# Kernel optimization log

Hardware: AMD Instinct MI355X
Metric: run time of the kernel (lower is better)

Reference implementation:

```python
import jax, jax.numpy as jnp
import numpy as np

HIDDEN = 4096
NUM_HEADS = 32
HEAD_DIM = 128
NUM_KV_HEADS = 8
KV_GROUPS = NUM_HEADS // NUM_KV_HEADS
ROPE_THETA = 10000.0
SEQ = 2048
BATCH = 1
NEG_INF = -1e9


def fake_quant_int8(x):
    """Per-tensor symmetric int8 fake quantization (absmax scale)."""
    scale = jnp.maximum(jnp.max(jnp.abs(x)) / 127.0, 1e-8)
    q = jnp.clip(jnp.round(x / scale), -127.0, 127.0) * scale
    # straight-through estimator (no-op in fwd-only, keeps code shared)
    return x + jax.lax.stop_gradient(q - x)


def rotate_half(x):
    x1, x2 = jnp.split(x, 2, axis=-1)
    return jnp.concatenate([-x2, x1], axis=-1)


def rope_cos_sin(position_ids):
    inv_freq = 1.0 / (ROPE_THETA ** (jnp.arange(0, HEAD_DIM, 2, dtype=jnp.float32) / HEAD_DIM))
    freqs = position_ids.astype(jnp.float32)[..., None] * inv_freq  # [B,S,HD/2]
    emb = jnp.concatenate([freqs, freqs], axis=-1)                  # [B,S,HD]
    return jnp.cos(emb), jnp.sin(emb)


def setup_inputs() -> dict:
    key = jax.random.key(0)
    k1, k2, k3, k4, k5 = jax.random.split(key, 5)
    hidden_states = jax.random.normal(k1, (BATCH, SEQ, HIDDEN), dtype=jnp.float32)
    causal = jnp.tril(jnp.ones((SEQ, SEQ), dtype=bool))
    attention_mask = jnp.where(causal, 0.0, NEG_INF).astype(jnp.float32)[None, None]  # [1,1,S,S]
    position_ids = jnp.arange(SEQ, dtype=jnp.int64 if jax.config.jax_enable_x64 else jnp.int32)[None, :]
    s = 0.02
    wq = jax.random.normal(k2, (NUM_HEADS * HEAD_DIM, HIDDEN), dtype=jnp.float32) * s
    wk = jax.random.normal(k3, (NUM_KV_HEADS * HEAD_DIM, HIDDEN), dtype=jnp.float32) * s
    wv = jax.random.normal(k4, (NUM_KV_HEADS * HEAD_DIM, HIDDEN), dtype=jnp.float32) * s
    wo = jax.random.normal(k5, (HIDDEN, NUM_HEADS * HEAD_DIM), dtype=jnp.float32) * s
    return {"hidden_states": hidden_states, "attention_mask": attention_mask,
            "position_ids": position_ids, "wq": wq, "wk": wk, "wv": wv, "wo": wo}


def reference(hidden_states, attention_mask, position_ids, wq, wk, wv, wo):
    B, S, _ = hidden_states.shape

    def qlinear(x, w):  # quantized linear: fake-quant act and weight, y = x @ w.T
        return fake_quant_int8(x) @ fake_quant_int8(w).T

    q = qlinear(hidden_states, wq).reshape(B, S, NUM_HEADS, HEAD_DIM).transpose(0, 2, 1, 3)
    k = qlinear(hidden_states, wk).reshape(B, S, NUM_KV_HEADS, HEAD_DIM).transpose(0, 2, 1, 3)
    v = qlinear(hidden_states, wv).reshape(B, S, NUM_KV_HEADS, HEAD_DIM).transpose(0, 2, 1, 3)

    cos, sin = rope_cos_sin(position_ids)      # [B,S,HD]
    cos, sin = cos[:, None], sin[:, None]      # [B,1,S,HD]
    q = q * cos + rotate_half(q) * sin
    k = k * cos + rotate_half(k) * sin

    # repeat_kv: GQA -> full heads
    k = jnp.repeat(k, KV_GROUPS, axis=1)
    v = jnp.repeat(v, KV_GROUPS, axis=1)

    # quantized QK^T
    scores = jnp.einsum('bhqd,bhkd->bhqk', fake_quant_int8(q), fake_quant_int8(k))
    scores = scores * (1.0 / np.sqrt(HEAD_DIM).astype(np.float32))
    scores = scores + attention_mask[:, :, :, :S]
    probs = jax.nn.softmax(scores.astype(jnp.float32), axis=-1).astype(q.dtype)
    # attention_dropout = 0.0 -> identity

    # quantized AV
    attn_out = jnp.einsum('bhqk,bhkd->bhqd', fake_quant_int8(probs), fake_quant_int8(v))
    attn_out = attn_out.transpose(0, 2, 1, 3).reshape(B, S, NUM_HEADS * HEAD_DIM)
    return qlinear(attn_out, wo)
```

## Files before the change

kernel.cpp:

```cpp
#include <hip/hip_runtime.h>
#include <stdint.h>

#define SEQ   2048
#define HID   4096
#define NH    32
#define NKV   8
#define KVDIM 1024
#define KVCAT 2048

typedef int v4i __attribute__((ext_vector_type(4)));

__device__ __forceinline__ float slot_scale(const unsigned* slots, int slot) {
    return fmaxf(__uint_as_float(slots[slot << 5]) / 127.0f, 1e-8f);
}

__device__ __forceinline__ int q8v(float x, float s) {
    int v = (int)rintf(x / s);
    return v < -127 ? -127 : (v > 127 ? 127 : v);
}

__device__ __forceinline__ float fexp2(float x) {
    float r; asm("v_exp_f32 %0, %1" : "=v"(r) : "v"(x)); return r;
}

__device__ __forceinline__ float amax4(const float* __restrict__ p, long v) {
    float4 x = *(const float4*)(p + v * 4);
    return fmaxf(fmaxf(fabsf(x.x), fabsf(x.y)), fmaxf(fabsf(x.z), fabsf(x.w)));
}

__device__ __forceinline__ void block_amax_atomic(float m, unsigned* slots, int slot) {
    __shared__ float sm[4];
    int lane = threadIdx.x & 63, w = threadIdx.x >> 6;
    for (int off = 32; off; off >>= 1) m = fmaxf(m, __shfl_xor(m, off, 64));
    if (lane == 0) sm[w] = m;
    __syncthreads();
    if (threadIdx.x == 0)
        atomicMax(slots + (slot << 5),
                  __float_as_uint(fmaxf(fmaxf(sm[0], sm[1]), fmaxf(sm[2], sm[3]))));
}

#define NV0 ((long)SEQ * HID / 4)
#define NV1 ((long)HID * HID / 4)
#define NV2 ((long)KVDIM * HID / 4)
__global__ void k_absmax5(const float* __restrict__ a0, const float* __restrict__ a1,
                          const float* __restrict__ a2, const float* __restrict__ a3,
                          const float* __restrict__ a4, unsigned* slots) {
    int b = blockIdx.x;
    const float* p; long n; int slot, lb, nb;
    if (b < 342)       { p = a0; n = NV0; slot = 0; lb = b;        nb = 342; }
    else if (b < 1025) { p = a1; n = NV1; slot = 1; lb = b - 342;  nb = 683; }
    else if (b < 1196) { p = a2; n = NV2; slot = 2; lb = b - 1025; nb = 171; }
    else if (b < 1367) { p = a3; n = NV2; slot = 3; lb = b - 1196; nb = 171; }
    else               { p = a4; n = NV1; slot = 4; lb = b - 1367; nb = 681; }
    long str = (long)nb * 256;
    float m = 0.f, m2 = 0.f;
    long v = (long)lb * 256 + threadIdx.x;
    for (; v + str < n; v += 2 * str) {
        m  = fmaxf(m,  amax4(p, v));
        m2 = fmaxf(m2, amax4(p, v + str));
    }
    if (v < n) m = fmaxf(m, amax4(p, v));
    block_amax_atomic(fmaxf(m, m2), slots, slot);
}

__device__ __forceinline__ void qstore4(const float* __restrict__ src, long v,
                                        int8_t* __restrict__ dst, float s) {
    float4 x = *(const float4*)(src + v * 4);
    unsigned pa = (unsigned)(uint8_t)(int8_t)q8v(x.x, s)
                | ((unsigned)(uint8_t)(int8_t)q8v(x.y, s) << 8)
                | ((unsigned)(uint8_t)(int8_t)q8v(x.z, s) << 16)
                | ((unsigned)(uint8_t)(int8_t)q8v(x.w, s) << 24);
    *(unsigned*)(dst + v * 4) = pa;
}

__global__ void k_quant4(const float* __restrict__ a0, const float* __restrict__ a1,
                         const float* __restrict__ a2, const float* __restrict__ a3,
                         int8_t* __restrict__ d0, int8_t* __restrict__ d1,
                         int8_t* __restrict__ d2, int8_t* __restrict__ d3,
                         const unsigned* __restrict__ slots) {
    int b = blockIdx.x;
    const float* p; int8_t* d; long n; int slot, lb, nb;
    if (b < 512)       { p = a0; d = d0; n = NV0; slot = 0; lb = b;        nb = 512; }
    else if (b < 1536) { p = a1; d = d1; n = NV1; slot = 1; lb = b - 512;  nb = 1024; }
    else if (b < 1792) { p = a2; d = d2; n = NV2; slot = 2; lb = b - 1536; nb = 256; }
    else               { p = a3; d = d3; n = NV2; slot = 3; lb = b - 1792; nb = 256; }
    float s = slot_scale(slots, slot);
    long str = (long)nb * 256;
    for (long v = (long)lb * 256 + threadIdx.x; v < n; v += str) qstore4(p, v, d, s);
}

__global__ void k_quant(const float* __restrict__ x, int8_t* __restrict__ q, long nvec,
                        int rshift, long cmaskv, long ld,
                        const unsigned* __restrict__ slots, int slot) {
    float s = slot_scale(slots, slot);
    for (long vid = blockIdx.x * (long)blockDim.x + threadIdx.x; vid < nvec;
         vid += (long)gridDim.x * blockDim.x) {
        long r = vid >> rshift;
        long c = (vid & cmaskv) << 2;
        float4 v = *(const float4*)(x + r * ld + c);
        unsigned pa = (unsigned)(uint8_t)(int8_t)q8v(v.x, s)
                    | ((unsigned)(uint8_t)(int8_t)q8v(v.y, s) << 8)
                    | ((unsigned)(uint8_t)(int8_t)q8v(v.z, s) << 16)
                    | ((unsigned)(uint8_t)(int8_t)q8v(v.w, s) << 24);
        *(unsigned*)(q + vid * 4) = pa;
    }
}

__global__ void k_ropetab(const int* __restrict__ pos, float* __restrict__ ct,
                          float* __restrict__ st) {
    int tid = blockIdx.x * blockDim.x + threadIdx.x;
    if (tid >= SEQ * 64) return;
    int i = tid & 63, s = tid >> 6;
    double inv = 1.0 / pow(10000.0, (double)((float)(2 * i) * (1.0f / 128.0f)));
    float invf = (float)inv;
    float angf = (float)pos[s] * invf;
    double a = (double)angf;
    ct[tid] = (float)cos(a);
    st[tid] = (float)sin(a);
}

__global__ void k_rope(float* __restrict__ x, long ld, int hbits, int total,
                       const float* __restrict__ ct, const float* __restrict__ st,
                       unsigned* slots, int slot) {
    float m = 0.f;
    for (int t = blockIdx.x * blockDim.x + threadIdx.x; t < total;
         t += gridDim.x * blockDim.x) {
        int i4 = t & 15;
        int h = (t >> 4) & ((1 << hbits) - 1);
        int s = t >> (4 + hbits);
        long base = (long)s * ld + h * 128 + i4 * 4;
        float4 a = *(float4*)(x + base);
        float4 b = *(float4*)(x + base + 64);
        float4 c = *(const float4*)(ct + s * 64 + i4 * 4);
        float4 sn = *(const float4*)(st + s * 64 + i4 * 4);
        float4 o0, o1;
        o0.x = a.x * c.x - b.x * sn.x;  o1.x = b.x * c.x + a.x * sn.x;
        o0.y = a.y * c.y - b.y * sn.y;  o1.y = b.y * c.y + a.y * sn.y;
        o0.z = a.z * c.z - b.z * sn.z;  o1.z = b.z * c.z + a.z * sn.z;
        o0.w = a.w * c.w - b.w * sn.w;  o1.w = b.w * c.w + a.w * sn.w;
        *(float4*)(x + base) = o0;
        *(float4*)(x + base + 64) = o1;
        m = fmaxf(m,
            fmaxf(fmaxf(fmaxf(fabsf(o0.x), fabsf(o0.y)), fmaxf(fabsf(o0.z), fabsf(o0.w))),
                  fmaxf(fmaxf(fabsf(o1.x), fabsf(o1.y)), fmaxf(fabsf(o1.z), fabsf(o1.w)))));
    }
    block_amax_atomic(m, slots, slot);
}

__global__ void k_transq(const float* __restrict__ src, long lds_, int8_t* __restrict__ dst,
                         long ldd, const unsigned* __restrict__ slots, int slot) {
    __shared__ float t[32][33];
    float s = slot_scale(slots, slot);
    int bx = blockIdx.x, by = blockIdx.y;
    int tid = threadIdx.x;
    int c = tid & 31, r0 = tid >> 5;
    #pragma unroll
    for (int j = 0; j < 4; j++) {
        int r = r0 + j * 8;
        t[r][c] = src[(long)(by * 32 + r) * lds_ + bx * 32 + c];
    }
    __syncthreads();
    int d = tid >> 3, k4 = (tid & 7) * 4;
    unsigned pa = 0;
    #pragma unroll
    for (int j = 0; j < 4; j++) {
        int iv = q8v(t[k4 + j][d], s);
        pa |= ((unsigned)(uint8_t)(int8_t)iv) << (8 * j);
    }
    *(unsigned*)(dst + (long)(bx * 32 + d) * ldd + by * 32 + k4) = pa;
}

__global__ __launch_bounds__(256) void k_gemm_i8(
    const int8_t* __restrict__ A, const int8_t* __restrict__ B, float* __restrict__ C,
    int M, int N, int K, unsigned* slots,
    int slotA, int slotB, int slotB2, int nsplit, int am_slot, int am_col0) {
    __shared__ int8_t As[128 * 128];
    __shared__ int8_t Bs[128 * 128];
    const v4i vzero = {0, 0, 0, 0};
    int tid = threadIdx.x, lane = tid & 63, wid = tid >> 6;
    int nbx = N >> 7;
    int nwg = gridDim.x, wg = blockIdx.x;
    int cpx = nwg >> 3;
    int swz = (wg & 7) * cpx + (wg >> 3);
    int bm = swz / nbx, bn = swz % nbx;
    long rowA0 = (long)bm * 128, colB0 = (long)bn * 128;
    int wrow = (wid >> 1) * 64, wcol = (wid & 1) * 64;
    v4i acc[4][4];
    #pragma unroll
    for (int m = 0; m < 4; m++)
        #pragma unroll
        for (int n = 0; n < 4; n++) acc[m][n] = vzero;
    for (int kt = 0; kt < K; kt += 128) {
        #pragma unroll
        for (int i = 0; i < 4; i++) {
            int chunk = tid + i * 256;
            int row = chunk >> 3, cc = chunk & 7;
            int sw = (cc ^ (row & 7)) * 16;
            v4i av = *(const v4i*)(A + (rowA0 + row) * K + kt + cc * 16);
            v4i bv = *(const v4i*)(B + (colB0 + row) * K + kt + cc * 16);
            *(v4i*)(As + row * 128 + sw) = av;
            *(v4i*)(Bs + row * 128 + sw) = bv;
        }
        __syncthreads();
        #pragma unroll
        for (int ks = 0; ks < 2; ks++) {
            v4i af[4], bf[4];
            #pragma unroll
            for (int m = 0; m < 4; m++) {
                int row = wrow + m * 16 + (lane & 15);
                af[m] = *(const v4i*)(As + row * 128 + (((ks * 4 + (lane >> 4)) ^ (row & 7)) * 16));
            }
            #pragma unroll
            for (int n = 0; n < 4; n++) {
                int row = wcol + n * 16 + (lane & 15);
                bf[n] = *(const v4i*)(Bs + row * 128 + (((ks * 4 + (lane >> 4)) ^ (row & 7)) * 16));
            }
            #pragma unroll
            for (int m = 0; m < 4; m++)
                #pragma unroll
                for (int n = 0; n < 4; n++)
                    acc[m][n] = __builtin_amdgcn_mfma_i32_16x16x64_i8(af[m], bf[n], acc[m][n], 0, 0, 0);
        }
        __syncthreads();
    }
    float sA = slot_scale(slots, slotA);
    float sB1 = slot_scale(slots, slotB);
    float sB2 = slot_scale(slots, slotB2);
    float am = 0.f;
    #pragma unroll
    for (int m = 0; m < 4; m++) {
        long row0 = rowA0 + wrow + m * 16 + ((lane >> 4) << 2);
        #pragma unroll
        for (int n = 0; n < 4; n++) {
            int col = (int)colB0 + wcol + n * 16 + (lane & 15);
            float sc = sA * ((col < nsplit) ? sB1 : sB2);
            float* cp = C + row0 * N + col;
            #pragma unroll
            for (int r = 0; r < 4; r++) {
                float val = sc * (float)acc[m][n][r];
                cp[(long)r * N] = val;
                if (col >= am_col0) am = fmaxf(am, fabsf(val));
            }
        }
    }
    if (am_slot >= 0) block_amax_atomic(am, slots, am_slot);
}

__global__ __launch_bounds__(256) void k_attn(
    const int8_t* __restrict__ Qq, const int8_t* __restrict__ Kq, const int8_t* __restrict__ Vtq,
    int* __restrict__ AO, unsigned* slots) {
    __shared__ int8_t Qs[64 * 128];
    __shared__ int8_t Ks[64 * 128];
    __shared__ int8_t Vs[128 * 64];
    __shared__ int smx[4];
    const v4i vzero = {0, 0, 0, 0};
    const int NEGS = -(1 << 29);
    int tid = threadIdx.x, lane = tid & 63, w = tid >> 6;
    int qlan = lane & 15, g = lane >> 4;
    int idx = blockIdx.x;
    int qb = 31 - (idx >> 5), h = idx & 31, kvh = h >> 2;
    float sq = slot_scale(slots, 5), sk = slot_scale(slots, 6);
    float c2 = sq * sk * 0.08838834764831845f * 1.4426950408889634f;
    #pragma unroll
    for (int i = 0; i < 2; i++) {
        int chunk = tid + i * 256;
        int row = chunk >> 3, cc = chunk & 7;
        v4i v = *(const v4i*)(Qq + (long)(qb * 64 + row) * HID + h * 128 + cc * 16);
        *(v4i*)(Qs + row * 128 + ((cc ^ (row & 7)) * 16)) = v;
    }
    __syncthreads();
    v4i aq[2];
    #pragma unroll
    for (int ks = 0; ks < 2; ks++) {
        int row = w * 16 + qlan;
        aq[ks] = *(const v4i*)(Qs + row * 128 + (((ks * 4 + g) ^ (row & 7)) * 16));
    }
    int mi = -(1 << 30);
    float l = 0.f;
    for (int kt = 0; kt <= qb; kt++) {
        __syncthreads();
        #pragma unroll
        for (int i = 0; i < 2; i++) {
            int chunk = tid + i * 256;
            int row = chunk >> 3, cc = chunk & 7;
            v4i v = *(const v4i*)(Kq + (long)(kt * 64 + row) * KVDIM + kvh * 128 + cc * 16);
            *(v4i*)(Ks + row * 128 + ((cc ^ (row & 7)) * 16)) = v;
        }
        __syncthreads();
        v4i sf[4] = {vzero, vzero, vzero, vzero};
        #pragma unroll
        for (int ks = 0; ks < 2; ks++)
            #pragma unroll
            for (int f = 0; f < 4; f++) {
                int row = f * 16 + qlan;
                v4i bk = *(const v4i*)(Ks + row * 128 + (((ks * 4 + g) ^ (row & 7)) * 16));
                sf[f] = __builtin_amdgcn_mfma_i32_16x16x64_i8(bk, aq[ks], sf[f], 0, 0, 0);
            }
        int qthr = qb * 64 + w * 16 + qlan - kt * 64;
        int sv[16];
        #pragma unroll
        for (int f = 0; f < 4; f++)
            #pragma unroll
            for (int r = 0; r < 4; r++) {
                int kl = f * 16 + g * 4 + r;
                sv[f * 4 + r] = (kl > qthr) ? NEGS : sf[f][r];
            }
        int tm = sv[0];
        #pragma unroll
        for (int e = 1; e < 16; e++) tm = tm > sv[e] ? tm : sv[e];
        tm = max(tm, __shfl_xor(tm, 16, 64));
        tm = max(tm, __shfl_xor(tm, 32, 64));
        int mn = tm > mi ? tm : mi;
        float esc = fexp2(c2 * (float)(mi - mn));
        float es = 0.f;
        #pragma unroll
        for (int e = 0; e < 16; e++) es += fexp2(c2 * (float)(sv[e] - mn));
        es += __shfl_xor(es, 16, 64);
        es += __shfl_xor(es, 32, 64);
        l = l * esc + es;
        mi = mn;
    }
    float invl = 127.0f / l;
    unsigned* Ps32 = (unsigned*)Qs;
    int pwr = w * 320;
    v4i of[8];
    #pragma unroll
    for (int nf = 0; nf < 8; nf++) of[nf] = vzero;
    for (int kt = 0; kt <= qb; kt++) {
        __syncthreads();
        #pragma unroll
        for (int i = 0; i < 2; i++) {
            int chunk = tid + i * 256;
            int row = chunk >> 3, cc = chunk & 7;
            v4i v = *(const v4i*)(Kq + (long)(kt * 64 + row) * KVDIM + kvh * 128 + cc * 16);
            *(v4i*)(Ks + row * 128 + ((cc ^ (row & 7)) * 16)) = v;
        }
        #pragma unroll
        for (int i = 0; i < 2; i++) {
            int chunk = tid + i * 256;
            int row = chunk >> 2, cc = chunk & 3;
            v4i v = *(const v4i*)(Vtq + (long)(kvh * 128 + row) * SEQ + kt * 64 + cc * 16);
            *(v4i*)(Vs + row * 64 + ((cc ^ (row & 3)) * 16)) = v;
        }
        __syncthreads();
        v4i sf[4] = {vzero, vzero, vzero, vzero};
        #pragma unroll
        for (int ks = 0; ks < 2; ks++)
            #pragma unroll
            for (int f = 0; f < 4; f++) {
                int row = f * 16 + qlan;
                v4i bk = *(const v4i*)(Ks + row * 128 + (((ks * 4 + g) ^ (row & 7)) * 16));
                sf[f] = __builtin_amdgcn_mfma_i32_16x16x64_i8(bk, aq[ks], sf[f], 0, 0, 0);
            }
        int qthr = qb * 64 + w * 16 + qlan - kt * 64;
        #pragma unroll
        for (int f = 0; f < 4; f++) {
            unsigned pk = 0;
            #pragma unroll
            for (int r = 0; r < 4; r++) {
                int kl = f * 16 + g * 4 + r;
                int s = (kl > qthr) ? NEGS : sf[f][r];
                float t = fexp2(c2 * (float)(s - mi));
                int pq = (int)rintf(t * invl);
                pk |= ((unsigned)pq) << (8 * r);
            }
            Ps32[pwr + (4 * f + g) * 20 + qlan] = pk;
        }
        int rb = pwr + 80 * g + qlan;
        v4i ap;
        ap[0] = (int)Ps32[rb];
        ap[1] = (int)Ps32[rb + 20];
        ap[2] = (int)Ps32[rb + 40];
        ap[3] = (int)Ps32[rb + 60];
        #pragma unroll
        for (int nf = 0; nf < 8; nf++) {
            int row = nf * 16 + qlan;
            v4i bv = *(const v4i*)(Vs + row * 64 + ((g ^ (row & 3)) * 16));
            of[nf] = __builtin_amdgcn_mfma_i32_16x16x64_i8(ap, bv, of[nf], 0, 0, 0);
        }
    }
    int mymax = 0;
    #pragma unroll
    for (int nf = 0; nf < 8; nf++)
        #pragma unroll
        for (int r = 0; r < 4; r++) {
            int val = of[nf][r];
            int av = val < 0 ? -val : val;
            mymax = av > mymax ? av : mymax;
            int qg = qb * 64 + w * 16 + 4 * g + r;
            AO[(long)qg * HID + h * 128 + nf * 16 + qlan] = val;
        }
    #pragma unroll
    for (int off = 1; off < 64; off <<= 1) {
        int o2 = __shfl_xor(mymax, off, 64);
        mymax = o2 > mymax ? o2 : mymax;
    }
    if (lane == 0) smx[w] = mymax;
    __syncthreads();
    if (tid == 0) {
        int mm = max(max(smx[0], smx[1]), max(smx[2], smx[3]));
        atomicMax(slots + (8 << 5), (unsigned)mm);
    }
}

__global__ void k_quant_ao(const int* __restrict__ a, int8_t* __restrict__ q, unsigned* slots) {
    float sv = slot_scale(slots, 7);
    float spv = (1.0f / 127.0f) * sv;
    float amax = spv * (float)(int)slots[8 << 5];
    float s = fmaxf(amax / 127.0f, 1e-8f);
    long nvec = (long)SEQ * HID / 4;
    for (long vid = blockIdx.x * (long)blockDim.x + threadIdx.x; vid < nvec;
         vid += (long)gridDim.x * blockDim.x) {
        int4 v = *(const int4*)(a + vid * 4);
        int a0 = q8v(spv * (float)v.x, s);
        int a1 = q8v(spv * (float)v.y, s);
        int a2 = q8v(spv * (float)v.z, s);
        int a3 = q8v(spv * (float)v.w, s);
        unsigned pa = (unsigned)(uint8_t)(int8_t)a0
                    | ((unsigned)(uint8_t)(int8_t)a1 << 8)
                    | ((unsigned)(uint8_t)(int8_t)a2 << 16)
                    | ((unsigned)(uint8_t)(int8_t)a3 << 24);
        *(unsigned*)(q + vid * 4) = pa;
    }
    if (blockIdx.x == 0 && threadIdx.x == 0) slots[9 << 5] = __float_as_uint(amax);
}

extern "C" void kernel_launch(void* const* d_in, const int* in_sizes, int n_in,
                              void* d_out, int out_size, void* d_ws, size_t ws_size,
                              hipStream_t stream) {
    (void)in_sizes; (void)n_in; (void)out_size;
    const float* hid = (const float*)d_in[0];
    const int* pos = (const int*)d_in[2];
    const float* wqp = (const float*)d_in[3];
    const float* wkp = (const float*)d_in[4];
    const float* wvp = (const float*)d_in[5];
    const float* wop = (const float*)d_in[6];
    float* out = (float*)d_out;
    char* ws = (char*)d_ws;

    size_t o = 0;
    auto alloc = [&](size_t sz) { size_t r = o; o += (sz + 255) & ~(size_t)255; return r; };
    unsigned* slots = (unsigned*)(ws + alloc(2048));
    int8_t* Xq   = (int8_t*)(ws + alloc((size_t)SEQ * HID));
    int8_t* Wqq  = (int8_t*)(ws + alloc((size_t)HID * HID));
    int8_t* Wkvq = (int8_t*)(ws + alloc((size_t)KVCAT * HID));
    float*  Qf   = (float*)(ws + alloc((size_t)SEQ * HID * 4));
    float*  KVf  = (float*)(ws + alloc((size_t)SEQ * KVCAT * 4));
    int8_t* Qq   = (int8_t*)(ws + alloc((size_t)SEQ * HID));
    int8_t* Kq   = (int8_t*)(ws + alloc((size_t)SEQ * KVDIM));
    int8_t* Vtq  = (int8_t*)(ws + alloc((size_t)KVDIM * SEQ));
    float*  ctab = (float*)(ws + alloc((size_t)SEQ * 64 * 4));
    float*  stab = (float*)(ws + alloc((size_t)SEQ * 64 * 4));
    if (ws_size < o) return;
    int8_t* Woq = Wqq;
    int*    AOint = (int*)Qf;
    int8_t* AOq = Xq;

    hipMemsetAsync(slots, 0, 2048, stream);
    k_ropetab<<<SEQ * 64 / 256, 256, 0, stream>>>(pos, ctab, stab);
    k_absmax5<<<2048, 256, 0, stream>>>(hid, wqp, wkp, wvp, wop, slots);
    k_quant4<<<2048, 256, 0, stream>>>(hid, wqp, wkp, wvp,
                                       Xq, Wqq, Wkvq, Wkvq + (size_t)KVDIM * HID, slots);
    k_gemm_i8<<<512, 256, 0, stream>>>(Xq, Wqq, Qf, SEQ, HID, HID, slots,
                                       0, 1, 1, 1 << 30, -1, 1 << 30);
    k_gemm_i8<<<256, 256, 0, stream>>>(Xq, Wkvq, KVf, SEQ, KVCAT, HID, slots,
                                       0, 2, 3, KVDIM, 7, KVDIM);
    const long CALL = 0x3FFFFFFFL;
    k_quant<<<2048, 256, 0, stream>>>(wop, Woq, (long)HID * HID / 4, 40, CALL, 0, slots, 4);
    k_rope<<<1024, 256, 0, stream>>>(Qf, HID, 5, SEQ * NH * 16, ctab, stab, slots, 5);
    k_rope<<<1024, 256, 0, stream>>>(KVf, KVCAT, 3, SEQ * NKV * 16, ctab, stab, slots, 6);
    k_quant<<<2048, 256, 0, stream>>>(Qf, Qq, (long)SEQ * HID / 4, 40, CALL, 0, slots, 5);
    k_quant<<<1024, 256, 0, stream>>>(KVf, Kq, (long)SEQ * KVDIM / 4, 8, 255, KVCAT, slots, 6);
    k_transq<<<dim3(32, 64), 256, 0, stream>>>(KVf + KVDIM, KVCAT, Vtq, SEQ, slots, 7);
    k_attn<<<1024, 256, 0, stream>>>(Qq, Kq, Vtq, AOint, slots);
    k_quant_ao<<<2048, 256, 0, stream>>>(AOint, AOq, slots);
    k_gemm_i8<<<512, 256, 0, stream>>>(AOq, Woq, out, SEQ, HID, HID, slots,
                                       9, 4, 4, 1 << 30, -1, 1 << 30);
}
```

Baseline: 350.8 us.

## Double-buffer GEMM and attention tiles with direct global-to-LDS async loads

Replaces the register-staged global-to-LDS copies in the int8 GEMM and the attention kernel with global_load_lds direct transfers. Tiles are double-buffered so the next K/V (or A/B) tile loads while MFMAs run on the current one. The attention kernel also applies the causal mask only on the diagonal tile and raises wave priority around the MFMA sections. This doubles LDS use (64 KB in the GEMM), which may lower occupancy, and relies on vmcnt waits for correctness.

```diff
diff --git a/kernel.cpp b/kernel.cpp
--- a/kernel.cpp
+++ b/kernel.cpp
@@ -9,6 +9,14 @@
 #define KVCAT 2048
 
 typedef int v4i __attribute__((ext_vector_type(4)));
+
+#define VMCNT0 asm volatile("s_waitcnt vmcnt(0)" ::: "memory")
+
+__device__ __forceinline__ void gload16(const void* g, void* l) {
+    __builtin_amdgcn_global_load_lds(
+        (const __attribute__((address_space(1))) void*)(uintptr_t)g,
+        (__attribute__((address_space(3))) void*)(uintptr_t)l, 16, 0, 0);
+}
 
 __device__ __forceinline__ float slot_scale(const unsigned* slots, int slot) {
     return fmaxf(__uint_as_float(slots[slot << 5]) / 127.0f, 1e-8f);
@@ -174,8 +182,8 @@
     const int8_t* __restrict__ A, const int8_t* __restrict__ B, float* __restrict__ C,
     int M, int N, int K, unsigned* slots,
     int slotA, int slotB, int slotB2, int nsplit, int am_slot, int am_col0) {
-    __shared__ int8_t As[128 * 128];
-    __shared__ int8_t Bs[128 * 128];
+    __shared__ int8_t As[2][128 * 128];
+    __shared__ int8_t Bs[2][128 * 128];
     const v4i vzero = {0, 0, 0, 0};
     int tid = threadIdx.x, lane = tid & 63, wid = tid >> 6;
     int nbx = N >> 7;
@@ -185,35 +193,36 @@
     int bm = swz / nbx, bn = swz % nbx;
     long rowA0 = (long)bm * 128, colB0 = (long)bn * 128;
     int wrow = (wid >> 1) * 64, wcol = (wid & 1) * 64;
+    int lr = lane >> 3;
+    int swc = ((lane & 7) ^ lr) * 16;
+    const int8_t* ga = A + (rowA0 + wid * 8 + lr) * (long)K + swc;
+    const int8_t* gb = B + (colB0 + wid * 8 + lr) * (long)K + swc;
     v4i acc[4][4];
     #pragma unroll
     for (int m = 0; m < 4; m++)
         #pragma unroll
         for (int n = 0; n < 4; n++) acc[m][n] = vzero;
-    for (int kt = 0; kt < K; kt += 128) {
+
+    auto STAGE = [&](int buf, int kt) {
         #pragma unroll
         for (int i = 0; i < 4; i++) {
-            int chunk = tid + i * 256;
-            int row = chunk >> 3, cc = chunk & 7;
-            int sw = (cc ^ (row & 7)) * 16;
-            v4i av = *(const v4i*)(A + (rowA0 + row) * K + kt + cc * 16);
-            v4i bv = *(const v4i*)(B + (colB0 + row) * K + kt + cc * 16);
-            *(v4i*)(As + row * 128 + sw) = av;
-            *(v4i*)(Bs + row * 128 + sw) = bv;
-        }
-        __syncthreads();
+            gload16(ga + kt + (long)(i * 32) * K, &As[buf][(wid * 8 + i * 32) * 128]);
+            gload16(gb + kt + (long)(i * 32) * K, &Bs[buf][(wid * 8 + i * 32) * 128]);
+        }
+    };
+    auto COMPUTE = [&](int buf) {
         #pragma unroll
         for (int ks = 0; ks < 2; ks++) {
             v4i af[4], bf[4];
             #pragma unroll
             for (int m = 0; m < 4; m++) {
                 int row = wrow + m * 16 + (lane & 15);
-                af[m] = *(const v4i*)(As + row * 128 + (((ks * 4 + (lane >> 4)) ^ (row & 7)) * 16));
+                af[m] = *(const v4i*)(&As[buf][row * 128 + (((ks * 4 + (lane >> 4)) ^ (row & 7)) * 16)]);
             }
             #pragma unroll
             for (int n = 0; n < 4; n++) {
                 int row = wcol + n * 16 + (lane & 15);
-                bf[n] = *(const v4i*)(Bs + row * 128 + (((ks * 4 + (lane >> 4)) ^ (row & 7)) * 16));
+                bf[n] = *(const v4i*)(&Bs[buf][row * 128 + (((ks * 4 + (lane >> 4)) ^ (row & 7)) * 16)]);
             }
             #pragma unroll
             for (int m = 0; m < 4; m++)
@@ -221,8 +230,21 @@
                 for (int n = 0; n < 4; n++)
                     acc[m][n] = __builtin_amdgcn_mfma_i32_16x16x64_i8(af[m], bf[n], acc[m][n], 0, 0, 0);
         }
+    };
+
+    STAGE(0, 0);
+    VMCNT0;
+    __syncthreads();
+    int nt = K >> 7, cur = 0;
+    for (int t = 0; t < nt - 1; t++) {
+        STAGE(cur ^ 1, (t + 1) << 7);
+        COMPUTE(cur);
+        VMCNT0;
         __syncthreads();
-    }
+        cur ^= 1;
+    }
+    COMPUTE(cur);
+
     float sA = slot_scale(slots, slotA);
     float sB1 = slot_scale(slots, slotB);
     float sB2 = slot_scale(slots, slotB2);
@@ -250,8 +272,8 @@
     const int8_t* __restrict__ Qq, const int8_t* __restrict__ Kq, const int8_t* __restrict__ Vtq,
     int* __restrict__ AO, unsigned* slots) {
     __shared__ int8_t Qs[64 * 128];
-    __shared__ int8_t Ks[64 * 128];
-    __shared__ int8_t Vs[128 * 64];
+    __shared__ int8_t Ks[2][64 * 128];
+    __shared__ int8_t Vs[2][128 * 64];
     __shared__ int smx[4];
     const v4i vzero = {0, 0, 0, 0};
     const int NEGS = -(1 << 29);
@@ -261,50 +283,69 @@
     int qb = 31 - (idx >> 5), h = idx & 31, kvh = h >> 2;
     float sq = slot_scale(slots, 5), sk = slot_scale(slots, 6);
     float c2 = sq * sk * 0.08838834764831845f * 1.4426950408889634f;
-    #pragma unroll
-    for (int i = 0; i < 2; i++) {
-        int chunk = tid + i * 256;
-        int row = chunk >> 3, cc = chunk & 7;
-        v4i v = *(const v4i*)(Qq + (long)(qb * 64 + row) * HID + h * 128 + cc * 16);
-        *(v4i*)(Qs + row * 128 + ((cc ^ (row & 7)) * 16)) = v;
-    }
+    int lr8 = lane >> 3;
+    int swc = ((lane & 7) ^ lr8) * 16;
+    int lr4 = lane >> 2;
+    int vswc = ((lane & 3) ^ (lr4 & 3)) * 16;
+    const int8_t* kbase = Kq + ((long)(w * 8 + lr8)) * KVDIM + kvh * 128 + swc;
+    const int8_t* vbase = Vtq + ((long)kvh * 128 + w * 16 + lr4) * SEQ + vswc;
+    auto STAGE_K = [&](int buf, int kt) {
+        #pragma unroll
+        for (int i = 0; i < 2; i++)
+            gload16(kbase + ((long)kt * 64 + i * 32) * KVDIM, &Ks[buf][(w * 8 + i * 32) * 128]);
+    };
+    auto STAGE_V = [&](int buf, int kt) {
+        #pragma unroll
+        for (int i = 0; i < 2; i++)
+            gload16(vbase + (long)(i * 64) * SEQ + kt * 64, &Vs[buf][(w * 16 + i * 64) * 64]);
+    };
+    {
+        const int8_t* qbase = Qq + ((long)qb * 64 + w * 8 + lr8) * HID + h * 128 + swc;
+        #pragma unroll
+        for (int i = 0; i < 2; i++)
+            gload16(qbase + (long)(i * 32) * HID, &Qs[(w * 8 + i * 32) * 128]);
+    }
+    STAGE_K(0, 0);
+    VMCNT0;
     __syncthreads();
     v4i aq[2];
     #pragma unroll
     for (int ks = 0; ks < 2; ks++) {
         int row = w * 16 + qlan;
-        aq[ks] = *(const v4i*)(Qs + row * 128 + (((ks * 4 + g) ^ (row & 7)) * 16));
+        aq[ks] = *(const v4i*)(&Qs[row * 128 + (((ks * 4 + g) ^ (row & 7)) * 16)]);
     }
     int mi = -(1 << 30);
     float l = 0.f;
+    int buf = 0;
     for (int kt = 0; kt <= qb; kt++) {
-        __syncthreads();
-        #pragma unroll
-        for (int i = 0; i < 2; i++) {
-            int chunk = tid + i * 256;
-            int row = chunk >> 3, cc = chunk & 7;
-            v4i v = *(const v4i*)(Kq + (long)(kt * 64 + row) * KVDIM + kvh * 128 + cc * 16);
-            *(v4i*)(Ks + row * 128 + ((cc ^ (row & 7)) * 16)) = v;
-        }
-        __syncthreads();
+        if (kt < qb) STAGE_K(buf ^ 1, kt + 1);
         v4i sf[4] = {vzero, vzero, vzero, vzero};
+        __builtin_amdgcn_s_setprio(1);
         #pragma unroll
         for (int ks = 0; ks < 2; ks++)
             #pragma unroll
             for (int f = 0; f < 4; f++) {
                 int row = f * 16 + qlan;
-                v4i bk = *(const v4i*)(Ks + row * 128 + (((ks * 4 + g) ^ (row & 7)) * 16));
+                v4i bk = *(const v4i*)(&Ks[buf][row * 128 + (((ks * 4 + g) ^ (row & 7)) * 16)]);
                 sf[f] = __builtin_amdgcn_mfma_i32_16x16x64_i8(bk, aq[ks], sf[f], 0, 0, 0);
             }
-        int qthr = qb * 64 + w * 16 + qlan - kt * 64;
+        __builtin_amdgcn_s_setprio(0);
         int sv[16];
-        #pragma unroll
-        for (int f = 0; f < 4; f++)
-            #pragma unroll
-            for (int r = 0; r < 4; r++) {
-                int kl = f * 16 + g * 4 + r;
-                sv[f * 4 + r] = (kl > qthr) ? NEGS : sf[f][r];
-            }
+        if (kt == qb) {
+            int qthr = w * 16 + qlan;
+            #pragma unroll
+            for (int f = 0; f < 4; f++)
+                #pragma unroll
+                for (int r = 0; r < 4; r++) {
+                    int kl = f * 16 + g * 4 + r;
+                    sv[f * 4 + r] = (kl > qthr) ? NEGS : sf[f][r];
+                }
+        } else {
+            #pragma unroll
+            for (int f = 0; f < 4; f++)
+                #pragma unroll
+                for (int r = 0; r < 4; r++) sv[f * 4 + r] = sf[f][r];
+        }
         int tm = sv[0];
         #pragma unroll
         for (int e = 1; e < 16; e++) tm = tm > sv[e] ? tm : sv[e];
@@ -319,6 +360,9 @@
         es += __shfl_xor(es, 32, 64);
         l = l * esc + es;
         mi = mn;
+        VMCNT0;
+        __syncthreads();
+        buf ^= 1;
     }
     float invl = 127.0f / l;
     unsigned* Ps32 = (unsigned*)Qs;
@@ -326,45 +370,51 @@
     v4i of[8];
     #pragma unroll
     for (int nf = 0; nf < 8; nf++) of[nf] = vzero;
+    STAGE_K(0, 0);
+    STAGE_V(0, 0);
+    VMCNT0;
+    __syncthreads();
+    buf = 0;
     for (int kt = 0; kt <= qb; kt++) {
-        __syncthreads();
-        #pragma unroll
-        for (int i = 0; i < 2; i++) {
-            int chunk = tid + i * 256;
-            int row = chunk >> 3, cc = chunk & 7;
-            v4i v = *(const v4i*)(Kq + (long)(kt * 64 + row) * KVDIM + kvh * 128 + cc * 16);
-            *(v4i*)(Ks + row * 128 + ((cc ^ (row & 7)) * 16)) = v;
-        }
-        #pragma unroll
-        for (int i = 0; i < 2; i++) {
-            int chunk = tid + i * 256;
-            int row = chunk >> 2, cc = chunk & 3;
-            v4i v = *(const v4i*)(Vtq + (long)(kvh * 128 + row) * SEQ + kt * 64 + cc * 16);
-            *(v4i*)(Vs + row * 64 + ((cc ^ (row & 3)) * 16)) = v;
-        }
-        __syncthreads();
+        if (kt < qb) { STAGE_K(buf ^ 1, kt + 1); STAGE_V(buf ^ 1, kt + 1); }
         v4i sf[4] = {vzero, vzero, vzero, vzero};
+        __builtin_amdgcn_s_setprio(1);
         #pragma unroll
         for (int ks = 0; ks < 2; ks++)
             #pragma unroll
             for (int f = 0; f < 4; f++) {
                 int row = f * 16 + qlan;
-                v4i bk = *(const v4i*)(Ks + row * 128 + (((ks * 4 + g) ^ (row & 7)) * 16));
+                v4i bk = *(const v4i*)(&Ks[buf][row * 128 + (((ks * 4 + g) ^ (row & 7)) * 16)]);
                 sf[f] = __builtin_amdgcn_mfma_i32_16x16x64_i8(bk, aq[ks], sf[f], 0, 0, 0);
             }
-        int qthr = qb * 64 + w * 16 + qlan - kt * 64;
-        #pragma unroll
-        for (int f = 0; f < 4; f++) {
-            unsigned pk = 0;
-            #pragma unroll
-            for (int r = 0; r < 4; r++) {
-                int kl = f * 16 + g * 4 + r;
-                int s = (kl > qthr) ? NEGS : sf[f][r];
-                float t = fexp2(c2 * (float)(s - mi));
-                int pq = (int)rintf(t * invl);
-                pk |= ((unsigned)pq) << (8 * r);
-            }
-            Ps32[pwr + (4 * f + g) * 20 + qlan] = pk;
+        __builtin_amdgcn_s_setprio(0);
+        if (kt == qb) {
+            int qthr = w * 16 + qlan;
+            #pragma unroll
+            for (int f = 0; f < 4; f++) {
+                unsigned pk = 0;
+                #pragma unroll
+                for (int r = 0; r < 4; r++) {
+                    int kl = f * 16 + g * 4 + r;
+                    int s = (kl > qthr) ? NEGS : sf[f][r];
+                    float t = fexp2(c2 * (float)(s - mi));
+                    int pq = (int)rintf(t * invl);
+                    pk |= ((unsigned)pq) << (8 * r);
+                }
+                Ps32[pwr + (4 * f + g) * 20 + qlan] = pk;
+            }
+        } else {
+            #pragma unroll
+            for (int f = 0; f < 4; f++) {
+                unsigned pk = 0;
+                #pragma unroll
+                for (int r = 0; r < 4; r++) {
+                    float t = fexp2(c2 * (float)(sf[f][r] - mi));
+                    int pq = (int)rintf(t * invl);
+                    pk |= ((unsigned)pq) << (8 * r);
+                }
+                Ps32[pwr + (4 * f + g) * 20 + qlan] = pk;
+            }
         }
         int rb = pwr + 80 * g + qlan;
         v4i ap;
@@ -372,12 +422,17 @@
         ap[1] = (int)Ps32[rb + 20];
         ap[2] = (int)Ps32[rb + 40];
         ap[3] = (int)Ps32[rb + 60];
+        __builtin_amdgcn_s_setprio(1);
         #pragma unroll
         for (int nf = 0; nf < 8; nf++) {
             int row = nf * 16 + qlan;
-            v4i bv = *(const v4i*)(Vs + row * 64 + ((g ^ (row & 3)) * 16));
+            v4i bv = *(const v4i*)(&Vs[buf][row * 64 + ((g ^ (row & 3)) * 16)]);
             of[nf] = __builtin_amdgcn_mfma_i32_16x16x64_i8(ap, bv, of[nf], 0, 0, 0);
         }
+        __builtin_amdgcn_s_setprio(0);
+        VMCNT0;
+        __syncthreads();
+        buf ^= 1;
     }
     int mymax = 0;
     #pragma unroll
```

Result: faster. 319.1 us (-9.0%).
